# Performance work log

Hardware: AMD Instinct MI355X
Metric: run time of the kernel (lower is better)

Reference implementation:

```python
import jax, jax.numpy as jnp
import numpy as np

LENGTH_OF_SIGNAL = 2560
OUTLIER_THRESHOLD = 3.0


def setup_inputs() -> dict:
    key = jax.random.key(0)
    inputs = jax.random.normal(key, (16384, 2560, 1), dtype=jnp.float32)
    return {"inputs": inputs}


def reference(inputs):
    # inputs: (B, S, 1). All stats reduce over the sequence axis (dim=1).
    B, S, _ = inputs.shape
    x = inputs[..., 0]  # (B, S)

    mean = jnp.mean(x, axis=1)                       # (B,)
    maximum = jnp.max(x, axis=1)
    minimum = jnp.min(x, axis=1)
    p2p = maximum - minimum
    rms = jnp.sqrt(jnp.mean(x * x, axis=1))
    var = jnp.var(x, axis=1, ddof=1)                 # torch.var is unbiased
    std = jnp.sqrt(var)                              # torch.std is unbiased

    centered = x - mean[:, None]
    skewness = jnp.mean(centered ** 3, axis=1) / (std ** 3)
    kurtosis = jnp.mean(centered ** 4, axis=1) / (std ** 4)

    abs_x = jnp.abs(x)
    abs_sum = jnp.sum(abs_x, axis=1)
    abs_max = jnp.max(abs_x, axis=1)
    shape_factor = rms * LENGTH_OF_SIGNAL / abs_sum
    impulse_factor = abs_max * LENGTH_OF_SIGNAL / abs_sum

    outliers = jnp.sum(
        (jnp.abs(centered) > OUTLIER_THRESHOLD * std[:, None]).astype(jnp.int32),
        axis=1,
    ).astype(jnp.float32)

    # zero-crossing rate on flattened (B, S) signal
    zcr = jnp.sum(
        (jnp.diff(jnp.sign(x), axis=1) != 0).astype(jnp.float32), axis=1
    ) / (2.0 * S)

    # Hjorth parameters (activity, mobility, complexity)
    d1 = jnp.diff(x, axis=1)
    d2 = jnp.diff(d1, axis=1)
    var_d1 = jnp.var(d1, axis=1, ddof=1)
    var_d2 = jnp.var(d2, axis=1, ddof=1)
    activity = var
    mobility = jnp.sqrt(var_d1 / var)
    complexity = jnp.sqrt(var_d2 / var_d1)

    stacked = jnp.stack(
        [mean, maximum, minimum, p2p, var, rms, skewness, kurtosis,
         shape_factor, impulse_factor, outliers, zcr,
         activity, mobility, complexity],
        axis=1,
    )  # (B, 15)
    return stacked
```

## Files before the change

### kernel.cpp

```cpp
#include <hip/hip_runtime.h>
#include <math.h>


constexpr int S_LEN = 2560;
constexpr int HALF  = 1280;

struct RowLds {
    double sum[2];
    double sq[2];
    float  sabs[2], vmax[2], vmin[2];
    float  nb0, nb1;
    float  ep0, ep1, ep2, ep3;
    float  c3s[2], c4s[2], s1q[2], s2q[2];
    float  outc[2], zcc[2];
};

__global__ __launch_bounds__(256)
void health_stats_kernel(const float* __restrict__ in, float* __restrict__ out) {
    __shared__ RowLds lds[2];

    const int lane = threadIdx.x & 63;
    const int wid  = threadIdx.x >> 6;
    const int hidx = wid & 1;
    const int rsl  = wid >> 1;
    const int row  = blockIdx.x * 2 + rsl;

    RowLds& L = lds[rsl];

    const float* rp = in + (size_t)row * S_LEN + hidx * HALF + lane * 4;

    float xr[20];
    float s8a = 0.f, q8a = 0.f;
    double sum = 0.0, sq = 0.0;
    float sabs = 0.f, vmax = -INFINITY, vmin = INFINITY;

#pragma unroll
    for (int k = 0; k < 5; ++k) {
        float4 a = *reinterpret_cast<const float4*>(rp + k * 256);
        xr[4*k+0]=a.x; xr[4*k+1]=a.y; xr[4*k+2]=a.z; xr[4*k+3]=a.w;
        float s4 = (a.x + a.y) + (a.z + a.w);
        float q4 = fmaf(a.x,a.x, fmaf(a.y,a.y, fmaf(a.z,a.z, a.w*a.w)));
        if ((k & 1) == 0) { s8a = s4; q8a = q4; }
        else              { sum += (double)(s8a + s4); sq += (double)(q8a + q4); }
        if (k == 4)       { sum += (double)s4; sq += (double)q4; }
        sabs += (fabsf(a.x)+fabsf(a.y)) + (fabsf(a.z)+fabsf(a.w));
        vmax = fmaxf(vmax, fmaxf(fmaxf(a.x,a.y), fmaxf(a.z,a.w)));
        vmin = fminf(vmin, fminf(fminf(a.x,a.y), fminf(a.z,a.w)));
    }

#pragma unroll
    for (int o = 32; o > 0; o >>= 1) {
        sum  += __shfl_xor(sum, o);
        sq   += __shfl_xor(sq, o);
        sabs += __shfl_xor(sabs, o);
        vmax  = fmaxf(vmax, __shfl_xor(vmax, o));
        vmin  = fminf(vmin, __shfl_xor(vmin, o));
    }

    if (lane == 0) {
        L.sum[hidx] = sum;  L.sq[hidx] = sq;
        L.sabs[hidx] = sabs; L.vmax[hidx] = vmax; L.vmin[hidx] = vmin;
        if (hidx == 0) { L.ep0 = xr[0]; L.ep1 = xr[1]; }
        else           { L.nb0 = xr[0]; L.nb1 = xr[1]; }
    }
    if (lane == 63 && hidx == 1) { L.ep2 = xr[18]; L.ep3 = xr[19]; }

    __syncthreads();

    const double tsum = L.sum[0] + L.sum[1];
    const double tsq  = L.sq[0]  + L.sq[1];
    const double mean = tsum * (1.0 / S_LEN);
    const double var  = (tsq - tsum * mean) * (1.0 / (S_LEN - 1));
    const double stdv = sqrt(var);
    const double thr  = 3.0 * stdv;

    const double bhi = mean + thr, blo = mean - thr;
    float bhi_f = (float)bhi;
    if ((double)bhi_f > bhi) bhi_f = __int_as_float(__float_as_int(bhi_f) - 1);
    float blo_f = (float)blo;
    if ((double)blo_f < blo) blo_f = __int_as_float(__float_as_int(blo_f) - 1);

    const float nbv0 = L.nb0, nbv1 = L.nb1;
    const float mf = (float)mean;

    float c3s = 0.f, c4s = 0.f, s1q = 0.f, s2q = 0.f;
    int outc = 0, zcc = 0;

#pragma unroll
    for (int k = 0; k < 5; ++k) {
        const float x0 = xr[4*k+0], x1 = xr[4*k+1], x2v = xr[4*k+2], x3 = xr[4*k+3];
        const int kn = (k == 4) ? 0 : (k + 1);
        float v0 = (lane == 0) ? xr[4*kn+0] : x0;
        float v1 = (lane == 0) ? xr[4*kn+1] : x1;
        float n0 = __shfl(v0, (lane + 1) & 63);
        float n1 = __shfl(v1, (lane + 1) & 63);
        if (k == 4 && lane == 63) { n0 = nbv0; n1 = nbv1; }

        const float c0 = x0 - mf, c1 = x1 - mf, c2 = x2v - mf, c3 = x3 - mf;
        const float q0 = c0*c0, q1 = c1*c1, q2 = c2*c2, q3 = c3*c3;
        c3s = fmaf(q0, c0, fmaf(q1, c1, fmaf(q2, c2, fmaf(q3, c3, c3s))));
        c4s = fmaf(q0, q0, fmaf(q1, q1, fmaf(q2, q2, fmaf(q3, q3, c4s))));

        outc += __popcll(__ballot(x0  > bhi_f || x0  < blo_f));
        outc += __popcll(__ballot(x1  > bhi_f || x1  < blo_f));
        outc += __popcll(__ballot(x2v > bhi_f || x2v < blo_f));
        outc += __popcll(__ballot(x3  > bhi_f || x3  < blo_f));

        const float d10 = x1 - x0, d11 = x2v - x1, d12 = x3 - x2v;
        const float d13 = n0 - x3, d14 = n1 - n0;
        const float e0 = d11 - d10, e1 = d12 - d11, e2 = d13 - d12, e3 = d14 - d13;

        const int b0 = __float_as_int(x0), b1 = __float_as_int(x1),
                  b2 = __float_as_int(x2v), b3 = __float_as_int(x3),
                  bn = __float_as_int(n0);
        zcc += __popcll(__ballot((b0 ^ b1) < 0));
        zcc += __popcll(__ballot((b1 ^ b2) < 0));
        zcc += __popcll(__ballot((b2 ^ b3) < 0));

        if (k < 4) {
            s1q = fmaf(d10, d10, fmaf(d11, d11, fmaf(d12, d12, fmaf(d13, d13, s1q))));
            s2q = fmaf(e0, e0, fmaf(e1, e1, fmaf(e2, e2, fmaf(e3, e3, s2q))));
            zcc += __popcll(__ballot((b3 ^ bn) < 0));
        } else {
            const bool ok = (hidx == 0) || (lane < 63);
            s1q = fmaf(d10, d10, fmaf(d11, d11, fmaf(d12, d12, s1q)));
            s1q += ok ? d13 * d13 : 0.f;
            s2q = fmaf(e0, e0, fmaf(e1, e1, s2q));
            s2q += ok ? e2 * e2 : 0.f;
            s2q += ok ? e3 * e3 : 0.f;
            zcc += __popcll(__ballot(((b3 ^ bn) < 0) && ok));
        }
    }

#pragma unroll
    for (int o = 32; o > 0; o >>= 1) {
        c3s += __shfl_xor(c3s, o);
        c4s += __shfl_xor(c4s, o);
        s1q += __shfl_xor(s1q, o);
        s2q += __shfl_xor(s2q, o);
    }

    if (lane == 0) {
        L.c3s[hidx] = c3s;  L.c4s[hidx] = c4s;
        L.s1q[hidx] = s1q;  L.s2q[hidx] = s2q;
        L.outc[hidx] = (float)outc;  L.zcc[hidx] = (float)zcc;
    }

    __syncthreads();

    if (hidx == 0 && lane == 0) {
        const float tabs = L.sabs[0] + L.sabs[1];
        const float tmax = fmaxf(L.vmax[0], L.vmax[1]);
        const float tmin = fminf(L.vmin[0], L.vmin[1]);
        const float c3t  = L.c3s[0] + L.c3s[1];
        const float c4t  = L.c4s[0] + L.c4s[1];
        const float s1qt = L.s1q[0] + L.s1q[1];
        const float s2qt = L.s2q[0] + L.s2q[1];
        const float outt = L.outc[0] + L.outc[1];
        const float zct  = L.zcc[0] + L.zcc[1];

        const double rms  = sqrt(tsq * (1.0 / S_LEN));
        const double m3   = (double)c3t * (1.0 / S_LEN);
        const double m4   = (double)c4t * (1.0 / S_LEN);
        const double skew = m3 / (var * stdv);
        const double kurt = m4 / (var * var);
        const float  amax = fmaxf(fabsf(tmax), fabsf(tmin));
        const double shape   = rms * (double)S_LEN / (double)tabs;
        const double impulse = (double)amax * (double)S_LEN / (double)tabs;
        const double s1 = (double)L.ep3 - (double)L.ep0;
        const double s2 = ((double)L.ep3 - (double)L.ep2) - ((double)L.ep1 - (double)L.ep0);
        const double var1 = ((double)s1qt - s1 * s1 * (1.0 / (S_LEN - 1))) * (1.0 / (S_LEN - 2));
        const double var2 = ((double)s2qt - s2 * s2 * (1.0 / (S_LEN - 2))) * (1.0 / (S_LEN - 3));

        float* o = out + (size_t)row * 15;
        o[0]  = (float)mean;
        o[1]  = tmax;
        o[2]  = tmin;
        o[3]  = tmax - tmin;
        o[4]  = (float)var;
        o[5]  = (float)rms;
        o[6]  = (float)skew;
        o[7]  = (float)kurt;
        o[8]  = (float)shape;
        o[9]  = (float)impulse;
        o[10] = outt;
        o[11] = zct * (1.0f / (2.0f * S_LEN));
        o[12] = (float)var;
        o[13] = (float)sqrt(var1 / var);
        o[14] = (float)sqrt(var2 / var1);
    }
}

extern "C" void kernel_launch(void* const* d_in, const int* in_sizes, int n_in,
                              void* d_out, int out_size, void* d_ws, size_t ws_size,
                              hipStream_t stream) {
    (void)in_sizes; (void)n_in; (void)d_ws; (void)ws_size; (void)out_size;
    const float* in = (const float*)d_in[0];
    float* out = (float*)d_out;
    health_stats_kernel<<<8192, 256, 0, stream>>>(in, out);
}
```

Baseline: 42.10 us.

## Split into pass1 plus finalize kernel with DPP reductions and packed math

Removes the second block barrier by having each wave write its partial statistics to a workspace, with a separate finalize kernel combining the halves and computing the 15 outputs. Wave reductions now use DPP row operations and readlane instead of shfl_xor. Sums and central moments use packed float2 FMAs, and zero crossings are counted from sign ballots XORed across elements. The cost is a second kernel launch plus a workspace write and read per row.

```diff
diff --git a/kernel.cpp b/kernel.cpp
--- a/kernel.cpp
+++ b/kernel.cpp
@@ -2,22 +2,59 @@
 #include <math.h>
 
 
+typedef float f32x2 __attribute__((ext_vector_type(2)));
+typedef float f32x4 __attribute__((ext_vector_type(4)));
+
 constexpr int S_LEN = 2560;
-constexpr int HALF  = 1280;
-
-struct RowLds {
-    double sum[2];
-    double sq[2];
-    float  sabs[2], vmax[2], vmin[2];
-    float  nb0, nb1;
-    float  ep0, ep1, ep2, ep3;
-    float  c3s[2], c4s[2], s1q[2], s2q[2];
-    float  outc[2], zcc[2];
-};
+constexpr int NROWS = 16384;
+
+#define DPP_ADD_F32(x, ctrl) do { \
+    int t_ = __builtin_amdgcn_update_dpp(0, __float_as_int(x), ctrl, 0xf, 0xf, false); \
+    x += __int_as_float(t_); } while (0)
+#define DPP_MAX_F32(x, ctrl) do { \
+    int t_ = __builtin_amdgcn_update_dpp(__float_as_int(x), __float_as_int(x), ctrl, 0xf, 0xf, false); \
+    x = fmaxf(x, __int_as_float(t_)); } while (0)
+#define DPP_MIN_F32(x, ctrl) do { \
+    int t_ = __builtin_amdgcn_update_dpp(__float_as_int(x), __float_as_int(x), ctrl, 0xf, 0xf, false); \
+    x = fminf(x, __int_as_float(t_)); } while (0)
+
+__device__ __forceinline__ float wave_sum_f32(float x) {
+    DPP_ADD_F32(x, 0x111); DPP_ADD_F32(x, 0x112); DPP_ADD_F32(x, 0x114);
+    DPP_ADD_F32(x, 0x118); DPP_ADD_F32(x, 0x142); DPP_ADD_F32(x, 0x143);
+    return x;
+}
+__device__ __forceinline__ float wave_max_f32(float x) {
+    DPP_MAX_F32(x, 0x111); DPP_MAX_F32(x, 0x112); DPP_MAX_F32(x, 0x114);
+    DPP_MAX_F32(x, 0x118); DPP_MAX_F32(x, 0x142); DPP_MAX_F32(x, 0x143);
+    return x;
+}
+__device__ __forceinline__ float wave_min_f32(float x) {
+    DPP_MIN_F32(x, 0x111); DPP_MIN_F32(x, 0x112); DPP_MIN_F32(x, 0x114);
+    DPP_MIN_F32(x, 0x118); DPP_MIN_F32(x, 0x142); DPP_MIN_F32(x, 0x143);
+    return x;
+}
+__device__ __forceinline__ double wave_sum_f64(double x) {
+#define DPP_ADD_F64(ctrl) do { \
+    long long b_ = __double_as_longlong(x); \
+    int lo_ = __builtin_amdgcn_update_dpp(0, (int)(b_ & 0xffffffffLL), ctrl, 0xf, 0xf, false); \
+    int hi_ = __builtin_amdgcn_update_dpp(0, (int)(b_ >> 32), ctrl, 0xf, 0xf, false); \
+    x += __longlong_as_double(((long long)hi_ << 32) | (unsigned int)lo_); } while (0)
+    DPP_ADD_F64(0x111); DPP_ADD_F64(0x112); DPP_ADD_F64(0x114);
+    DPP_ADD_F64(0x118); DPP_ADD_F64(0x142); DPP_ADD_F64(0x143);
+#undef DPP_ADD_F64
+    return x;
+}
+__device__ __forceinline__ double readlane_f64(double x, int l) {
+    long long b = __double_as_longlong(x);
+    int lo = __builtin_amdgcn_readlane((int)(b & 0xffffffffLL), l);
+    int hi = __builtin_amdgcn_readlane((int)(b >> 32), l);
+    return __longlong_as_double(((long long)hi << 32) | (unsigned int)lo);
+}
 
 __global__ __launch_bounds__(256)
-void health_stats_kernel(const float* __restrict__ in, float* __restrict__ out) {
-    __shared__ RowLds lds[2];
+void health_pass1(const float* __restrict__ in, float* __restrict__ ws) {
+    __shared__ double Lsum[4], Lsq[4];
+    __shared__ float  Lnb[2][2];
 
     const int lane = threadIdx.x & 63;
     const int wid  = threadIdx.x >> 6;
@@ -25,102 +62,97 @@
     const int rsl  = wid >> 1;
     const int row  = blockIdx.x * 2 + rsl;
 
-    RowLds& L = lds[rsl];
-
-    const float* rp = in + (size_t)row * S_LEN + hidx * HALF + lane * 4;
-
-    float xr[20];
-    float s8a = 0.f, q8a = 0.f;
-    double sum = 0.0, sq = 0.0;
+    const f32x4* rp = reinterpret_cast<const f32x4*>(in)
+                    + (size_t)row * (S_LEN / 4) + hidx * (1280 / 4) + lane;
+
+    f32x4 X[5];
+#pragma unroll
+    for (int k = 0; k < 5; ++k) X[k] = rp[k * 64];
+
+    f32x2 sp = {0.f, 0.f}, qp = {0.f, 0.f};
     float sabs = 0.f, vmax = -INFINITY, vmin = INFINITY;
-
 #pragma unroll
     for (int k = 0; k < 5; ++k) {
-        float4 a = *reinterpret_cast<const float4*>(rp + k * 256);
-        xr[4*k+0]=a.x; xr[4*k+1]=a.y; xr[4*k+2]=a.z; xr[4*k+3]=a.w;
-        float s4 = (a.x + a.y) + (a.z + a.w);
-        float q4 = fmaf(a.x,a.x, fmaf(a.y,a.y, fmaf(a.z,a.z, a.w*a.w)));
-        if ((k & 1) == 0) { s8a = s4; q8a = q4; }
-        else              { sum += (double)(s8a + s4); sq += (double)(q8a + q4); }
-        if (k == 4)       { sum += (double)s4; sq += (double)q4; }
-        sabs += (fabsf(a.x)+fabsf(a.y)) + (fabsf(a.z)+fabsf(a.w));
-        vmax = fmaxf(vmax, fmaxf(fmaxf(a.x,a.y), fmaxf(a.z,a.w)));
-        vmin = fminf(vmin, fminf(fminf(a.x,a.y), fminf(a.z,a.w)));
-    }
-
-#pragma unroll
-    for (int o = 32; o > 0; o >>= 1) {
-        sum  += __shfl_xor(sum, o);
-        sq   += __shfl_xor(sq, o);
-        sabs += __shfl_xor(sabs, o);
-        vmax  = fmaxf(vmax, __shfl_xor(vmax, o));
-        vmin  = fminf(vmin, __shfl_xor(vmin, o));
-    }
+        f32x2 lo = __builtin_shufflevector(X[k], X[k], 0, 1);
+        f32x2 hi = __builtin_shufflevector(X[k], X[k], 2, 3);
+        sp += lo + hi;
+        qp = __builtin_elementwise_fma(lo, lo, qp);
+        qp = __builtin_elementwise_fma(hi, hi, qp);
+        sabs += (fabsf(X[k][0]) + fabsf(X[k][1])) + (fabsf(X[k][2]) + fabsf(X[k][3]));
+        vmax = fmaxf(vmax, fmaxf(fmaxf(X[k][0], X[k][1]), fmaxf(X[k][2], X[k][3])));
+        vmin = fminf(vmin, fminf(fminf(X[k][0], X[k][1]), fminf(X[k][2], X[k][3])));
+    }
+
+    const double sum_l = (double)sp.x + (double)sp.y;
+    const double sq_l  = (double)qp.x + (double)qp.y;
+    const double sum_u = readlane_f64(wave_sum_f64(sum_l), 63);
+    const double sq_u  = readlane_f64(wave_sum_f64(sq_l), 63);
 
     if (lane == 0) {
-        L.sum[hidx] = sum;  L.sq[hidx] = sq;
-        L.sabs[hidx] = sabs; L.vmax[hidx] = vmax; L.vmin[hidx] = vmin;
-        if (hidx == 0) { L.ep0 = xr[0]; L.ep1 = xr[1]; }
-        else           { L.nb0 = xr[0]; L.nb1 = xr[1]; }
-    }
-    if (lane == 63 && hidx == 1) { L.ep2 = xr[18]; L.ep3 = xr[19]; }
-
+        Lsum[wid] = sum_u;  Lsq[wid] = sq_u;
+        if (hidx == 1) { Lnb[rsl][0] = X[0][0]; Lnb[rsl][1] = X[0][1]; }
+    }
     __syncthreads();
-
-    const double tsum = L.sum[0] + L.sum[1];
-    const double tsq  = L.sq[0]  + L.sq[1];
+    const double tsum = Lsum[rsl * 2] + Lsum[rsl * 2 + 1];
+    const double tsq  = Lsq[rsl * 2]  + Lsq[rsl * 2 + 1];
+
     const double mean = tsum * (1.0 / S_LEN);
     const double var  = (tsq - tsum * mean) * (1.0 / (S_LEN - 1));
     const double stdv = sqrt(var);
     const double thr  = 3.0 * stdv;
-
     const double bhi = mean + thr, blo = mean - thr;
     float bhi_f = (float)bhi;
     if ((double)bhi_f > bhi) bhi_f = __int_as_float(__float_as_int(bhi_f) - 1);
     float blo_f = (float)blo;
     if ((double)blo_f < blo) blo_f = __int_as_float(__float_as_int(blo_f) - 1);
 
-    const float nbv0 = L.nb0, nbv1 = L.nb1;
+    const float nbv0 = Lnb[rsl][0], nbv1 = Lnb[rsl][1];
     const float mf = (float)mean;
-
-    float c3s = 0.f, c4s = 0.f, s1q = 0.f, s2q = 0.f;
+    const f32x2 nmf2 = {-mf, -mf};
+
+    f32x2 c3p = {0.f, 0.f}, c4p = {0.f, 0.f};
+    float s1q = 0.f, s2q = 0.f;
     int outc = 0, zcc = 0;
+    const unsigned long long tail_ok = (hidx == 0) ? ~0ULL : 0x7FFFFFFFFFFFFFFFULL;
 
 #pragma unroll
     for (int k = 0; k < 5; ++k) {
-        const float x0 = xr[4*k+0], x1 = xr[4*k+1], x2v = xr[4*k+2], x3 = xr[4*k+3];
+        const float x0 = X[k][0], x1 = X[k][1], x2v = X[k][2], x3 = X[k][3];
         const int kn = (k == 4) ? 0 : (k + 1);
-        float v0 = (lane == 0) ? xr[4*kn+0] : x0;
-        float v1 = (lane == 0) ? xr[4*kn+1] : x1;
+        float v0 = (lane == 0) ? X[kn][0] : x0;
+        float v1 = (lane == 0) ? X[kn][1] : x1;
         float n0 = __shfl(v0, (lane + 1) & 63);
         float n1 = __shfl(v1, (lane + 1) & 63);
         if (k == 4 && lane == 63) { n0 = nbv0; n1 = nbv1; }
 
-        const float c0 = x0 - mf, c1 = x1 - mf, c2 = x2v - mf, c3 = x3 - mf;
-        const float q0 = c0*c0, q1 = c1*c1, q2 = c2*c2, q3 = c3*c3;
-        c3s = fmaf(q0, c0, fmaf(q1, c1, fmaf(q2, c2, fmaf(q3, c3, c3s))));
-        c4s = fmaf(q0, q0, fmaf(q1, q1, fmaf(q2, q2, fmaf(q3, q3, c4s))));
+        f32x2 lo = __builtin_shufflevector(X[k], X[k], 0, 1);
+        f32x2 hi = __builtin_shufflevector(X[k], X[k], 2, 3);
+        f32x2 cl = lo + nmf2, ch = hi + nmf2;
+        f32x2 ql = cl * cl,  qh = ch * ch;
+        c3p = __builtin_elementwise_fma(ql, cl, c3p);
+        c3p = __builtin_elementwise_fma(qh, ch, c3p);
+        c4p = __builtin_elementwise_fma(ql, ql, c4p);
+        c4p = __builtin_elementwise_fma(qh, qh, c4p);
 
         outc += __popcll(__ballot(x0  > bhi_f || x0  < blo_f));
         outc += __popcll(__ballot(x1  > bhi_f || x1  < blo_f));
         outc += __popcll(__ballot(x2v > bhi_f || x2v < blo_f));
         outc += __popcll(__ballot(x3  > bhi_f || x3  < blo_f));
 
+        const unsigned long long m0 = __ballot(x0  < 0.f);
+        const unsigned long long m1 = __ballot(x1  < 0.f);
+        const unsigned long long m2 = __ballot(x2v < 0.f);
+        const unsigned long long m3 = __ballot(x3  < 0.f);
+        const unsigned long long mn = __ballot(n0  < 0.f);
+        zcc += __popcll(m0 ^ m1) + __popcll(m1 ^ m2) + __popcll(m2 ^ m3);
+        zcc += __popcll((m3 ^ mn) & ((k == 4) ? tail_ok : ~0ULL));
+
         const float d10 = x1 - x0, d11 = x2v - x1, d12 = x3 - x2v;
         const float d13 = n0 - x3, d14 = n1 - n0;
         const float e0 = d11 - d10, e1 = d12 - d11, e2 = d13 - d12, e3 = d14 - d13;
-
-        const int b0 = __float_as_int(x0), b1 = __float_as_int(x1),
-                  b2 = __float_as_int(x2v), b3 = __float_as_int(x3),
-                  bn = __float_as_int(n0);
-        zcc += __popcll(__ballot((b0 ^ b1) < 0));
-        zcc += __popcll(__ballot((b1 ^ b2) < 0));
-        zcc += __popcll(__ballot((b2 ^ b3) < 0));
-
         if (k < 4) {
             s1q = fmaf(d10, d10, fmaf(d11, d11, fmaf(d12, d12, fmaf(d13, d13, s1q))));
             s2q = fmaf(e0, e0, fmaf(e1, e1, fmaf(e2, e2, fmaf(e3, e3, s2q))));
-            zcc += __popcll(__ballot((b3 ^ bn) < 0));
         } else {
             const bool ok = (hidx == 0) || (lane < 63);
             s1q = fmaf(d10, d10, fmaf(d11, d11, fmaf(d12, d12, s1q)));
@@ -128,74 +160,103 @@
             s2q = fmaf(e0, e0, fmaf(e1, e1, s2q));
             s2q += ok ? e2 * e2 : 0.f;
             s2q += ok ? e3 * e3 : 0.f;
-            zcc += __popcll(__ballot(((b3 ^ bn) < 0) && ok));
         }
     }
 
-#pragma unroll
-    for (int o = 32; o > 0; o >>= 1) {
-        c3s += __shfl_xor(c3s, o);
-        c4s += __shfl_xor(c4s, o);
-        s1q += __shfl_xor(s1q, o);
-        s2q += __shfl_xor(s2q, o);
-    }
-
-    if (lane == 0) {
-        L.c3s[hidx] = c3s;  L.c4s[hidx] = c4s;
-        L.s1q[hidx] = s1q;  L.s2q[hidx] = s2q;
-        L.outc[hidx] = (float)outc;  L.zcc[hidx] = (float)zcc;
-    }
-
-    __syncthreads();
-
-    if (hidx == 0 && lane == 0) {
-        const float tabs = L.sabs[0] + L.sabs[1];
-        const float tmax = fmaxf(L.vmax[0], L.vmax[1]);
-        const float tmin = fminf(L.vmin[0], L.vmin[1]);
-        const float c3t  = L.c3s[0] + L.c3s[1];
-        const float c4t  = L.c4s[0] + L.c4s[1];
-        const float s1qt = L.s1q[0] + L.s1q[1];
-        const float s2qt = L.s2q[0] + L.s2q[1];
-        const float outt = L.outc[0] + L.outc[1];
-        const float zct  = L.zcc[0] + L.zcc[1];
-
-        const double rms  = sqrt(tsq * (1.0 / S_LEN));
-        const double m3   = (double)c3t * (1.0 / S_LEN);
-        const double m4   = (double)c4t * (1.0 / S_LEN);
-        const double skew = m3 / (var * stdv);
-        const double kurt = m4 / (var * var);
-        const float  amax = fmaxf(fabsf(tmax), fabsf(tmin));
-        const double shape   = rms * (double)S_LEN / (double)tabs;
-        const double impulse = (double)amax * (double)S_LEN / (double)tabs;
-        const double s1 = (double)L.ep3 - (double)L.ep0;
-        const double s2 = ((double)L.ep3 - (double)L.ep2) - ((double)L.ep1 - (double)L.ep0);
-        const double var1 = ((double)s1qt - s1 * s1 * (1.0 / (S_LEN - 1))) * (1.0 / (S_LEN - 2));
-        const double var2 = ((double)s2qt - s2 * s2 * (1.0 / (S_LEN - 2))) * (1.0 / (S_LEN - 3));
-
-        float* o = out + (size_t)row * 15;
-        o[0]  = (float)mean;
-        o[1]  = tmax;
-        o[2]  = tmin;
-        o[3]  = tmax - tmin;
-        o[4]  = (float)var;
-        o[5]  = (float)rms;
-        o[6]  = (float)skew;
-        o[7]  = (float)kurt;
-        o[8]  = (float)shape;
-        o[9]  = (float)impulse;
-        o[10] = outt;
-        o[11] = zct * (1.0f / (2.0f * S_LEN));
-        o[12] = (float)var;
-        o[13] = (float)sqrt(var1 / var);
-        o[14] = (float)sqrt(var2 / var1);
-    }
+    float sabs_t = wave_sum_f32(sabs);
+    float c3_t   = wave_sum_f32(c3p.x + c3p.y);
+    float c4_t   = wave_sum_f32(c4p.x + c4p.y);
+    float s1q_t  = wave_sum_f32(s1q);
+    float s2q_t  = wave_sum_f32(s2q);
+    float vmax_t = wave_max_f32(vmax);
+    float vmin_t = wave_min_f32(vmin);
+
+    float ep_a, ep_b;
+    if (hidx == 0) {
+        ep_a = __int_as_float(__builtin_amdgcn_readlane(__float_as_int(X[0][0]), 0));
+        ep_b = __int_as_float(__builtin_amdgcn_readlane(__float_as_int(X[0][1]), 0));
+    } else {
+        ep_a = X[4][2];  ep_b = X[4][3];
+    }
+
+    if (lane == 63) {
+        double2* Wd = reinterpret_cast<double2*>(ws);
+        f32x4*   Wf = reinterpret_cast<f32x4*>(ws);
+        double2 dsum; dsum.x = sum_u; dsum.y = sq_u;
+        Wd[(size_t)hidx * NROWS + row] = dsum;
+        const size_t b = (size_t)(2 + hidx * 3) * NROWS + row;
+        Wf[b]             = f32x4{sabs_t, vmax_t, vmin_t, c3_t};
+        Wf[b + NROWS]     = f32x4{c4_t, s1q_t, s2q_t, (float)outc};
+        Wf[b + 2 * NROWS] = f32x4{(float)zcc, ep_a, ep_b, 0.f};
+    }
+}
+
+__global__ __launch_bounds__(256)
+void health_finalize(const float* __restrict__ ws, float* __restrict__ out) {
+    const int row = blockIdx.x * 256 + threadIdx.x;
+    const double2* Wd = reinterpret_cast<const double2*>(ws);
+    const f32x4*   Wf = reinterpret_cast<const f32x4*>(ws);
+
+    const double2 s0 = Wd[row], s1 = Wd[NROWS + row];
+    const f32x4 a0 = Wf[2 * NROWS + row], a1 = Wf[3 * NROWS + row], a2 = Wf[4 * NROWS + row];
+    const f32x4 b0 = Wf[5 * NROWS + row], b1 = Wf[6 * NROWS + row], b2 = Wf[7 * NROWS + row];
+
+    const double tsum = s0.x + s1.x;
+    const double tsq  = s0.y + s1.y;
+    const double mean = tsum * (1.0 / S_LEN);
+    const double var  = (tsq - tsum * mean) * (1.0 / (S_LEN - 1));
+    const double stdv = sqrt(var);
+
+    const float tabs = a0[0] + b0[0];
+    const float tmax = fmaxf(a0[1], b0[1]);
+    const float tmin = fminf(a0[2], b0[2]);
+    const float c3t  = a0[3] + b0[3];
+    const float c4t  = a1[0] + b1[0];
+    const float s1qt = a1[1] + b1[1];
+    const float s2qt = a1[2] + b1[2];
+    const float outt = a1[3] + b1[3];
+    const float zct  = a2[0] + b2[0];
+    const float ep0 = a2[1], ep1 = a2[2];
+    const float ep2 = b2[1], ep3 = b2[2];
+
+    const double rms  = sqrt(tsq * (1.0 / S_LEN));
+    const double m3   = (double)c3t * (1.0 / S_LEN);
+    const double m4   = (double)c4t * (1.0 / S_LEN);
+    const double skew = m3 / (var * stdv);
+    const double kurt = m4 / (var * var);
+    const float  amax = fmaxf(fabsf(tmax), fabsf(tmin));
+    const double shape   = rms * (double)S_LEN / (double)tabs;
+    const double impulse = (double)amax * (double)S_LEN / (double)tabs;
+    const double sd1 = (double)ep3 - (double)ep0;
+    const double sd2 = ((double)ep3 - (double)ep2) - ((double)ep1 - (double)ep0);
+    const double var1 = ((double)s1qt - sd1 * sd1 * (1.0 / (S_LEN - 1))) * (1.0 / (S_LEN - 2));
+    const double var2 = ((double)s2qt - sd2 * sd2 * (1.0 / (S_LEN - 2))) * (1.0 / (S_LEN - 3));
+
+    float* o = out + (size_t)row * 15;
+    o[0]  = (float)mean;
+    o[1]  = tmax;
+    o[2]  = tmin;
+    o[3]  = tmax - tmin;
+    o[4]  = (float)var;
+    o[5]  = (float)rms;
+    o[6]  = (float)skew;
+    o[7]  = (float)kurt;
+    o[8]  = (float)shape;
+    o[9]  = (float)impulse;
+    o[10] = outt;
+    o[11] = zct * (1.0f / (2.0f * S_LEN));
+    o[12] = (float)var;
+    o[13] = (float)sqrt(var1 / var);
+    o[14] = (float)sqrt(var2 / var1);
 }
 
 extern "C" void kernel_launch(void* const* d_in, const int* in_sizes, int n_in,
                               void* d_out, int out_size, void* d_ws, size_t ws_size,
                               hipStream_t stream) {
-    (void)in_sizes; (void)n_in; (void)d_ws; (void)ws_size; (void)out_size;
+    (void)in_sizes; (void)n_in; (void)ws_size; (void)out_size;
     const float* in = (const float*)d_in[0];
     float* out = (float*)d_out;
-    health_stats_kernel<<<8192, 256, 0, stream>>>(in, out);
-}
+    float* ws  = (float*)d_ws;
+    health_pass1<<<8192, 256, 0, stream>>>(in, ws);
+    health_finalize<<<64, 256, 0, stream>>>(ws, out);
+}
```

Result: faster. 39.90 us (-5.2%).
